# Kernel optimization log

Hardware: AMD Instinct MI355X
Metric: run time of the kernel (lower is better)

Reference implementation:

```python
import jax, jax.numpy as jnp
import numpy as np

GRID_SIZE = 5
SPLINE_ORDER = 3
NUM_BASIS = GRID_SIZE + SPLINE_ORDER  # 8
GRID = jnp.linspace(-1.0, 1.0, GRID_SIZE + 2 * SPLINE_ORDER + 1)  # [12]
EPS = 1e-6


def bspline_basis(x):
    """Iterative Cox-de Boor. x: [...]; returns [..., NUM_BASIS]."""
    xe = x[..., None]
    # order-0 indicator basis: [..., G-1]
    B = ((xe >= GRID[:-1]) & (xe < GRID[1:])).astype(x.dtype)
    for k in range(1, SPLINE_ORDER + 1):
        nb = B.shape[-1] - 1
        g_i = GRID[:nb]
        g_i1 = GRID[1:1 + nb]
        g_ik = GRID[k:k + nb]
        g_ik1 = GRID[k + 1:k + 1 + nb]
        dl = g_ik - g_i
        dr = g_ik1 - g_i1
        left = jnp.where(dl > EPS, (xe - g_i) / jnp.where(dl > EPS, dl, 1.0), 0.0) * B[..., :nb]
        right = jnp.where(dr > EPS, (g_ik1 - xe) / jnp.where(dr > EPS, dr, 1.0), 0.0) * B[..., 1:nb + 1]
        B = left + right
    return B[..., :NUM_BASIS]


def setup_inputs() -> dict:
    key = jax.random.key(0)
    k1, k2 = jax.random.split(key)
    x = jax.random.normal(k1, (8192, 512), dtype=jnp.float32)
    spline_coeffs = jax.random.normal(k2, (512, 512, NUM_BASIS), dtype=jnp.float32) * 0.1
    return {"x": x, "spline_coeffs": spline_coeffs}


def reference(x, spline_coeffs):
    xn = jnp.tanh(x)                       # [B, in]
    basis = bspline_basis(xn)              # [B, in, K]
    # output[b, o] = sum_{i,k} coeffs[o, i, k] * basis[b, i, k]
    return jnp.einsum('bik,oik->bo', basis, spline_coeffs)
```

## Files before the change

### kernel.cpp

```cpp
#include <hip/hip_runtime.h>
#include <hip/hip_bf16.h>
#include <stdint.h>


#define M_TOTAL 8192
#define N_DIM   512
#define K_DIM   4096
#define BM 128
#define BN 128
#define BK 64
#define BUF_BYTES ((BM + BN) * BK * 2)

typedef __attribute__((ext_vector_type(8))) short short8;
typedef __attribute__((ext_vector_type(4))) float f32x4;

typedef const __attribute__((address_space(1))) uint32_t ga_u32;
typedef __attribute__((address_space(3))) uint32_t ls_u32;

__device__ __forceinline__ void gload_lds16(const void* g, void* l) {
  __builtin_amdgcn_global_load_lds((ga_u32*)(uintptr_t)g,
                                   (ls_u32*)(uint32_t)(uintptr_t)l, 16, 0, 0);
}

__device__ __forceinline__ unsigned short f2bf(float f) {
  uint32_t u = __builtin_bit_cast(uint32_t, f);
  u = (u + 0x7FFFu + ((u >> 16) & 1u)) >> 16;
  return (unsigned short)u;
}

__global__ __launch_bounds__(256) void basis_kernel(const float* __restrict__ x,
                                                    __hip_bfloat16* __restrict__ A,
                                                    int total) {
  int idx = blockIdx.x * 256 + threadIdx.x;
  if (idx >= total) return;
  float xv = x[idx];
  xv = fminf(15.f, fmaxf(-15.f, xv));
  float e = __expf(2.0f * xv);
  float t = (e - 1.0f) * __builtin_amdgcn_rcpf(e + 1.0f);
  float uf = (t + 1.0f) * 5.5f;
  int c = (int)uf;
  c = c > 10 ? 10 : c;
  float u  = uf - (float)c;
  float u2 = u * u, u3 = u2 * u;
  float om = 1.0f - u;
  float w0 = om * om * om * (1.0f / 6.0f);
  float w1 = (3.0f * u3 - 6.0f * u2 + 4.0f) * (1.0f / 6.0f);
  float w2 = (-3.0f * u3 + 3.0f * u2 + 3.0f * u + 1.0f) * (1.0f / 6.0f);
  float w3 = u3 * (1.0f / 6.0f);
  union { unsigned short us[8]; int4 v; } pk;
#pragma unroll
  for (int j = 0; j < 8; ++j) {
    int i = j - c + 3;
    float v = (i == 0) ? w0 : (i == 1) ? w1 : (i == 2) ? w2 : (i == 3) ? w3 : 0.f;
    pk.us[j] = f2bf(v);
  }
  reinterpret_cast<int4*>(A)[idx] = pk.v;
}

__global__ __launch_bounds__(256) void cvt_kernel(const float* __restrict__ c,
                                                  __hip_bfloat16* __restrict__ Bt,
                                                  int total8) {
  int idx = blockIdx.x * 256 + threadIdx.x;
  if (idx >= total8) return;
  const float4* cp = reinterpret_cast<const float4*>(c) + (size_t)idx * 2;
  float4 a = cp[0], b = cp[1];
  union { unsigned short us[8]; int4 v; } pack;
  pack.us[0] = f2bf(a.x); pack.us[1] = f2bf(a.y);
  pack.us[2] = f2bf(a.z); pack.us[3] = f2bf(a.w);
  pack.us[4] = f2bf(b.x); pack.us[5] = f2bf(b.y);
  pack.us[6] = f2bf(b.z); pack.us[7] = f2bf(b.w);
  reinterpret_cast<int4*>(Bt)[idx] = pack.v;
}

__global__ __launch_bounds__(256) void gemm_kernel(
    const __hip_bfloat16* __restrict__ A,
    const __hip_bfloat16* __restrict__ Bt,
    float* __restrict__ C) {
  __shared__ __hip_bfloat16 lds[2 * (BM + BN) * BK];

  const int tid   = threadIdx.x;
  const int wid   = tid >> 6;
  const int lane  = tid & 63;
  const int quad  = lane >> 4;
  const int l16   = lane & 15;
  const int waveM = wid >> 1;
  const int waveN = wid & 1;

  int b = blockIdx.x, mt, nt;
  int nm = gridDim.x >> 2;
  if ((nm & 7) == 0) {
    int xcd = b & 7, q = b >> 3, per = nm >> 3;
    mt = xcd * per + (q >> 2);
    nt = q & 3;
  } else { mt = b >> 2; nt = b & 3; }
  const int m0 = mt * BM;
  const int n0 = nt * BN;

  uint32_t aGlob[4], bGlob[4], sLds[4];
#pragma unroll
  for (int t = 0; t < 4; ++t) {
    int s = t * 256 + tid;
    int row = s >> 3, p = s & 7, cc = p ^ (row & 7);
    aGlob[t] = (uint32_t)(m0 + row) * (uint32_t)K_DIM + (uint32_t)cc * 8u;
    bGlob[t] = (uint32_t)(n0 + row) * (uint32_t)K_DIM + (uint32_t)cc * 8u;
    sLds[t]  = (uint32_t)s * 16u;
  }

  uint32_t aOff[2][4], bOff[2][4];
#pragma unroll
  for (int kk = 0; kk < 2; ++kk) {
    int c = kk * 4 + quad;
#pragma unroll
    for (int mi = 0; mi < 4; ++mi) {
      int row = waveM * 64 + mi * 16 + l16;
      aOff[kk][mi] = (uint32_t)(row * 8 + (c ^ (row & 7))) * 16u;
    }
#pragma unroll
    for (int ni = 0; ni < 4; ++ni) {
      int row = waveN * 64 + ni * 16 + l16;
      bOff[kk][ni] = (uint32_t)(BM * BK * 2) + (uint32_t)(row * 8 + (c ^ (row & 7))) * 16u;
    }
  }

  char* ldsc = (char*)lds;

  f32x4 acc[4][4];
#pragma unroll
  for (int mi = 0; mi < 4; ++mi)
#pragma unroll
    for (int ni = 0; ni < 4; ++ni)
      acc[mi][ni] = (f32x4){0.f, 0.f, 0.f, 0.f};

  const int NT = K_DIM / BK;

#pragma unroll
  for (int t = 0; t < 4; ++t) {
    gload_lds16(A + aGlob[t], ldsc + sLds[t]);
    gload_lds16(Bt + bGlob[t], ldsc + BM * BK * 2 + sLds[t]);
  }

  for (int it = 0; it < NT; ++it) {
    const int cur = it & 1;
    char* bufc = ldsc + cur * BUF_BYTES;
    __syncthreads();
    if (it + 1 < NT) {
      char* bufn = ldsc + (1 - cur) * BUF_BYTES;
      uint32_t kt = (uint32_t)(it + 1) * BK;
#pragma unroll
      for (int t = 0; t < 4; ++t) {
        gload_lds16(A + aGlob[t] + kt, bufn + sLds[t]);
        gload_lds16(Bt + bGlob[t] + kt, bufn + BM * BK * 2 + sLds[t]);
      }
    }
#pragma unroll
    for (int kk = 0; kk < 2; ++kk) {
      short8 af[4], bf[4];
#pragma unroll
      for (int mi = 0; mi < 4; ++mi)
        af[mi] = *reinterpret_cast<const short8*>(bufc + aOff[kk][mi]);
#pragma unroll
      for (int ni = 0; ni < 4; ++ni)
        bf[ni] = *reinterpret_cast<const short8*>(bufc + bOff[kk][ni]);
#pragma unroll
      for (int mi = 0; mi < 4; ++mi)
#pragma unroll
        for (int ni = 0; ni < 4; ++ni)
          acc[mi][ni] = __builtin_amdgcn_mfma_f32_16x16x32_bf16(
              af[mi], bf[ni], acc[mi][ni], 0, 0, 0);
    }
  }

#pragma unroll
  for (int mi = 0; mi < 4; ++mi) {
#pragma unroll
    for (int ni = 0; ni < 4; ++ni) {
      int col = n0 + waveN * 64 + ni * 16 + l16;
#pragma unroll
      for (int r = 0; r < 4; ++r) {
        int row = m0 + waveM * 64 + mi * 16 + quad * 4 + r;
        C[(size_t)row * N_DIM + col] = acc[mi][ni][r];
      }
    }
  }
}

extern "C" void kernel_launch(void* const* d_in, const int* in_sizes, int n_in,
                              void* d_out, int out_size, void* d_ws, size_t ws_size,
                              hipStream_t stream) {
  const float* x    = (const float*)d_in[0];
  const float* coef = (const float*)d_in[1];
  float* out = (float*)d_out;

  const size_t BT_BYTES = (size_t)N_DIM * K_DIM * 2;
  __hip_bfloat16* Bt = (__hip_bfloat16*)d_ws;
  __hip_bfloat16* A  = (__hip_bfloat16*)((char*)d_ws + BT_BYTES);

  size_t avail = (ws_size > BT_BYTES) ? ws_size - BT_BYTES : 0;
  long maxRows = (long)(avail / ((size_t)K_DIM * 2));
  maxRows = (maxRows / BM) * BM;
  if (maxRows > M_TOTAL) maxRows = M_TOTAL;
  if (maxRows < BM) maxRows = BM;

  const int total8 = N_DIM * K_DIM / 8;
  cvt_kernel<<<(total8 + 255) / 256, 256, 0, stream>>>(coef, Bt, total8);

  for (long r0 = 0; r0 < M_TOTAL; r0 += maxRows) {
    long rows  = (M_TOTAL - r0 < maxRows) ? (M_TOTAL - r0) : maxRows;
    long total = rows * 512;
    basis_kernel<<<(int)((total + 255) / 256), 256, 0, stream>>>(
        x + r0 * 512, A, (int)total);
    dim3 grid((unsigned)((rows / BM) * (N_DIM / BN)));
    gemm_kernel<<<grid, 256, 0, stream>>>(A, Bt, out + r0 * N_DIM);
  }
}
```

Baseline: 144.6 us.

## Fuse B-spline basis generation into GEMM with split-K wave groups

Drops the separate basis kernel and its 64 MB bf16 A matrix round trip. Each GEMM block now computes the tanh and cubic B-spline weights directly into LDS from x and places them with 64-bit shifts. The block becomes 512 threads split into two K-halves, each with its own double-buffered LDS region, and the two partial sums are reduced through LDS before the store. The cost is more ALU work inside the GEMM loop, a 128 KB LDS footprint per block that limits occupancy, and loss of the workspace-chunking fallback.

```diff
diff --git a/kernel.cpp b/kernel.cpp
--- a/kernel.cpp
+++ b/kernel.cpp
@@ -9,7 +9,9 @@
 #define BM 128
 #define BN 128
 #define BK 64
-#define BUF_BYTES ((BM + BN) * BK * 2)
+#define NT_HALF 32
+#define GRP_LDS 65536
+#define BUF_HALF 32768
 
 typedef __attribute__((ext_vector_type(8))) short short8;
 typedef __attribute__((ext_vector_type(4))) float f32x4;
@@ -22,39 +24,33 @@
                                    (ls_u32*)(uint32_t)(uintptr_t)l, 16, 0, 0);
 }
 
-__device__ __forceinline__ unsigned short f2bf(float f) {
+__device__ __forceinline__ uint32_t f2bf(float f) {
   uint32_t u = __builtin_bit_cast(uint32_t, f);
-  u = (u + 0x7FFFu + ((u >> 16) & 1u)) >> 16;
-  return (unsigned short)u;
-}
-
-__global__ __launch_bounds__(256) void basis_kernel(const float* __restrict__ x,
-                                                    __hip_bfloat16* __restrict__ A,
-                                                    int total) {
-  int idx = blockIdx.x * 256 + threadIdx.x;
-  if (idx >= total) return;
-  float xv = x[idx];
+  return (u + 0x7FFFu + ((u >> 16) & 1u)) >> 16;
+}
+
+__device__ __forceinline__ void basis_slots(float xv, uint32_t o[4]) {
   xv = fminf(15.f, fmaxf(-15.f, xv));
-  float e = __expf(2.0f * xv);
-  float t = (e - 1.0f) * __builtin_amdgcn_rcpf(e + 1.0f);
+  float e  = __expf(2.0f * xv);
+  float t  = (e - 1.0f) * __builtin_amdgcn_rcpf(e + 1.0f);
   float uf = (t + 1.0f) * 5.5f;
-  int c = (int)uf;
-  c = c > 10 ? 10 : c;
+  int   c  = (int)uf;  c = c > 10 ? 10 : c;
   float u  = uf - (float)c;
-  float u2 = u * u, u3 = u2 * u;
-  float om = 1.0f - u;
+  float u2 = u * u, u3 = u2 * u, om = 1.0f - u;
   float w0 = om * om * om * (1.0f / 6.0f);
   float w1 = (3.0f * u3 - 6.0f * u2 + 4.0f) * (1.0f / 6.0f);
   float w2 = (-3.0f * u3 + 3.0f * u2 + 3.0f * u + 1.0f) * (1.0f / 6.0f);
   float w3 = u3 * (1.0f / 6.0f);
-  union { unsigned short us[8]; int4 v; } pk;
-#pragma unroll
-  for (int j = 0; j < 8; ++j) {
-    int i = j - c + 3;
-    float v = (i == 0) ? w0 : (i == 1) ? w1 : (i == 2) ? w2 : (i == 3) ? w3 : 0.f;
-    pk.us[j] = f2bf(v);
-  }
-  reinterpret_cast<int4*>(A)[idx] = pk.v;
+  uint32_t p01 = f2bf(w0) | (f2bf(w1) << 16);
+  uint32_t p23 = f2bf(w2) | (f2bf(w3) << 16);
+  uint64_t W = (uint64_t)p01 | ((uint64_t)p23 << 32);
+  int d = c - 3;
+  uint64_t lo = (d < 0) ? (W >> ((-d) * 16))
+              : ((d < 4) ? (W << (d * 16)) : 0ull);
+  uint64_t hi = (d <= 0) ? 0ull
+              : ((d < 4) ? (W >> ((4 - d) * 16)) : (W << ((d - 4) * 16)));
+  o[0] = (uint32_t)lo; o[1] = (uint32_t)(lo >> 32);
+  o[2] = (uint32_t)hi; o[3] = (uint32_t)(hi >> 32);
 }
 
 __global__ __launch_bounds__(256) void cvt_kernel(const float* __restrict__ c,
@@ -64,46 +60,46 @@
   if (idx >= total8) return;
   const float4* cp = reinterpret_cast<const float4*>(c) + (size_t)idx * 2;
   float4 a = cp[0], b = cp[1];
-  union { unsigned short us[8]; int4 v; } pack;
-  pack.us[0] = f2bf(a.x); pack.us[1] = f2bf(a.y);
-  pack.us[2] = f2bf(a.z); pack.us[3] = f2bf(a.w);
-  pack.us[4] = f2bf(b.x); pack.us[5] = f2bf(b.y);
-  pack.us[6] = f2bf(b.z); pack.us[7] = f2bf(b.w);
-  reinterpret_cast<int4*>(Bt)[idx] = pack.v;
-}
-
-__global__ __launch_bounds__(256) void gemm_kernel(
-    const __hip_bfloat16* __restrict__ A,
+  union { unsigned short us[8]; int4 v; } pk;
+  pk.us[0] = f2bf(a.x); pk.us[1] = f2bf(a.y);
+  pk.us[2] = f2bf(a.z); pk.us[3] = f2bf(a.w);
+  pk.us[4] = f2bf(b.x); pk.us[5] = f2bf(b.y);
+  pk.us[6] = f2bf(b.z); pk.us[7] = f2bf(b.w);
+  reinterpret_cast<int4*>(Bt)[idx] = pk.v;
+}
+
+__global__ __launch_bounds__(512, 2) void fused_kernel(
+    const float* __restrict__ x,
     const __hip_bfloat16* __restrict__ Bt,
     float* __restrict__ C) {
-  __shared__ __hip_bfloat16 lds[2 * (BM + BN) * BK];
+  __shared__ char lds[2 * GRP_LDS];
 
   const int tid   = threadIdx.x;
   const int wid   = tid >> 6;
   const int lane  = tid & 63;
   const int quad  = lane >> 4;
   const int l16   = lane & 15;
-  const int waveM = wid >> 1;
-  const int waveN = wid & 1;
-
-  int b = blockIdx.x, mt, nt;
-  int nm = gridDim.x >> 2;
-  if ((nm & 7) == 0) {
-    int xcd = b & 7, q = b >> 3, per = nm >> 3;
-    mt = xcd * per + (q >> 2);
-    nt = q & 3;
-  } else { mt = b >> 2; nt = b & 3; }
-  const int m0 = mt * BM;
-  const int n0 = nt * BN;
-
-  uint32_t aGlob[4], bGlob[4], sLds[4];
+  const int kgrp  = wid >> 2;
+  const int w2    = wid & 3;
+  const int waveM = w2 >> 1, waveN = w2 & 1;
+  const int tg    = tid & 255;
+
+  int b = blockIdx.x;
+  int mt = (b & 7) * 8 + ((b >> 3) >> 2);
+  int nt = (b >> 3) & 3;
+  const int m0 = mt * BM, n0 = nt * BN;
+
+  char* grp = lds + kgrp * GRP_LDS;
+
+  uint32_t bGlob[4], sOff[4], xBase[4], aWr[4];
 #pragma unroll
   for (int t = 0; t < 4; ++t) {
-    int s = t * 256 + tid;
-    int row = s >> 3, p = s & 7, cc = p ^ (row & 7);
-    aGlob[t] = (uint32_t)(m0 + row) * (uint32_t)K_DIM + (uint32_t)cc * 8u;
-    bGlob[t] = (uint32_t)(n0 + row) * (uint32_t)K_DIM + (uint32_t)cc * 8u;
-    sLds[t]  = (uint32_t)s * 16u;
+    int s = t * 256 + tg, row = s >> 3, p = s & 7;
+    sOff[t]  = (uint32_t)s * 16u;
+    bGlob[t] = (uint32_t)(n0 + row) * K_DIM + (uint32_t)(p ^ (row & 7)) * 8u
+             + (uint32_t)kgrp * 2048u;
+    xBase[t] = (uint32_t)(m0 + row) * 512u + (uint32_t)kgrp * 256u + (uint32_t)p;
+    aWr[t]   = (uint32_t)(row * 8 + (p ^ (row & 7))) * 16u;
   }
 
   uint32_t aOff[2][4], bOff[2][4];
@@ -118,11 +114,9 @@
 #pragma unroll
     for (int ni = 0; ni < 4; ++ni) {
       int row = waveN * 64 + ni * 16 + l16;
-      bOff[kk][ni] = (uint32_t)(BM * BK * 2) + (uint32_t)(row * 8 + (c ^ (row & 7))) * 16u;
-    }
-  }
-
-  char* ldsc = (char*)lds;
+      bOff[kk][ni] = 16384u + (uint32_t)(row * 8 + (c ^ (row & 7))) * 16u;
+    }
+  }
 
   f32x4 acc[4][4];
 #pragma unroll
@@ -131,25 +125,29 @@
     for (int ni = 0; ni < 4; ++ni)
       acc[mi][ni] = (f32x4){0.f, 0.f, 0.f, 0.f};
 
-  const int NT = K_DIM / BK;
-
+#pragma unroll
+  for (int t = 0; t < 4; ++t)
+    gload_lds16(Bt + bGlob[t], grp + 16384 + sOff[t]);
 #pragma unroll
   for (int t = 0; t < 4; ++t) {
-    gload_lds16(A + aGlob[t], ldsc + sLds[t]);
-    gload_lds16(Bt + bGlob[t], ldsc + BM * BK * 2 + sLds[t]);
-  }
-
-  for (int it = 0; it < NT; ++it) {
+    uint32_t o[4]; basis_slots(x[xBase[t]], o);
+    *reinterpret_cast<int4*>(grp + aWr[t]) = make_int4(o[0], o[1], o[2], o[3]);
+  }
+
+  for (int it = 0; it < NT_HALF; ++it) {
     const int cur = it & 1;
-    char* bufc = ldsc + cur * BUF_BYTES;
+    char* bufc = grp + cur * BUF_HALF;
     __syncthreads();
-    if (it + 1 < NT) {
-      char* bufn = ldsc + (1 - cur) * BUF_BYTES;
-      uint32_t kt = (uint32_t)(it + 1) * BK;
+    if (it + 1 < NT_HALF) {
+      char* bufn = grp + (1 - cur) * BUF_HALF;
+      uint32_t kOff = (uint32_t)(it + 1) * 64u;
+#pragma unroll
+      for (int t = 0; t < 4; ++t)
+        gload_lds16(Bt + bGlob[t] + kOff, bufn + 16384 + sOff[t]);
 #pragma unroll
       for (int t = 0; t < 4; ++t) {
-        gload_lds16(A + aGlob[t] + kt, bufn + sLds[t]);
-        gload_lds16(Bt + bGlob[t] + kt, bufn + BM * BK * 2 + sLds[t]);
+        uint32_t o[4]; basis_slots(x[xBase[t] + (uint32_t)(it + 1) * 8u], o);
+        *reinterpret_cast<int4*>(bufn + aWr[t]) = make_int4(o[0], o[1], o[2], o[3]);
       }
     }
 #pragma unroll
@@ -170,15 +168,33 @@
     }
   }
 
-#pragma unroll
-  for (int mi = 0; mi < 4; ++mi) {
-#pragma unroll
-    for (int ni = 0; ni < 4; ++ni) {
-      int col = n0 + waveN * 64 + ni * 16 + l16;
-#pragma unroll
-      for (int r = 0; r < 4; ++r) {
-        int row = m0 + waveM * 64 + mi * 16 + quad * 4 + r;
-        C[(size_t)row * N_DIM + col] = acc[mi][ni][r];
+  __syncthreads();
+  if (kgrp == 1) {
+#pragma unroll
+    for (int mi = 0; mi < 4; ++mi)
+#pragma unroll
+      for (int ni = 0; ni < 4; ++ni) {
+        int f = mi * 4 + ni;
+        *reinterpret_cast<f32x4*>(lds + w2 * 16384 + f * 1024 + lane * 16) =
+            acc[mi][ni];
+      }
+  }
+  __syncthreads();
+  if (kgrp == 0) {
+#pragma unroll
+    for (int mi = 0; mi < 4; ++mi) {
+#pragma unroll
+      for (int ni = 0; ni < 4; ++ni) {
+        int f = mi * 4 + ni;
+        f32x4 other = *reinterpret_cast<f32x4*>(
+            lds + w2 * 16384 + f * 1024 + lane * 16);
+        f32x4 s = acc[mi][ni] + other;
+        int col = n0 + waveN * 64 + ni * 16 + l16;
+#pragma unroll
+        for (int r = 0; r < 4; ++r) {
+          int row = m0 + waveM * 64 + mi * 16 + quad * 4 + r;
+          C[(size_t)row * N_DIM + col] = s[r];
+        }
       }
     }
   }
@@ -191,25 +207,10 @@
   const float* coef = (const float*)d_in[1];
   float* out = (float*)d_out;
 
-  const size_t BT_BYTES = (size_t)N_DIM * K_DIM * 2;
   __hip_bfloat16* Bt = (__hip_bfloat16*)d_ws;
-  __hip_bfloat16* A  = (__hip_bfloat16*)((char*)d_ws + BT_BYTES);
-
-  size_t avail = (ws_size > BT_BYTES) ? ws_size - BT_BYTES : 0;
-  long maxRows = (long)(avail / ((size_t)K_DIM * 2));
-  maxRows = (maxRows / BM) * BM;
-  if (maxRows > M_TOTAL) maxRows = M_TOTAL;
-  if (maxRows < BM) maxRows = BM;
 
   const int total8 = N_DIM * K_DIM / 8;
   cvt_kernel<<<(total8 + 255) / 256, 256, 0, stream>>>(coef, Bt, total8);
 
-  for (long r0 = 0; r0 < M_TOTAL; r0 += maxRows) {
-    long rows  = (M_TOTAL - r0 < maxRows) ? (M_TOTAL - r0) : maxRows;
-    long total = rows * 512;
-    basis_kernel<<<(int)((total + 255) / 256), 256, 0, stream>>>(
-        x + r0 * 512, A, (int)total);
-    dim3 grid((unsigned)((rows / BM) * (N_DIM / BN)));
-    gemm_kernel<<<grid, 256, 0, stream>>>(A, Bt, out + r0 * N_DIM);
-  }
-}
+  fused_kernel<<<(M_TOTAL / BM) * (N_DIM / BN), 512, 0, stream>>>(x, Bt, out);
+}
```

Measured after the change: 147.6 us. 2.1% more time.
